# Kernel optimization log

Measured on AMD Instinct MI355X. Metric: run time of the kernel, lower is better.

## Reference

```python
import jax, jax.numpy as jnp
import numpy as np


def setup_inputs() -> dict:
    key = jax.random.key(0)
    k1, k2 = jax.random.split(key, 2)
    B, N, D = 8, 2048, 1024
    x = jax.random.normal(k1, (B, N, D), dtype=jnp.float32)
    # Linear(D, 3D): weight stored as [in, out] for x @ W
    W_qkv = jax.random.normal(k2, (D, 3 * D), dtype=jnp.float32) * (D ** -0.5)
    b_qkv = jnp.zeros((3 * D,), dtype=jnp.float32)
    return {"x": x, "W_qkv": W_qkv, "b_qkv": b_qkv}


def reference(x, W_qkv, b_qkv):
    D = x.shape[-1]
    scale = D ** -0.5
    qkv = x @ W_qkv + b_qkv                      # [B, N, 3D]
    q, k, v = jnp.split(qkv, 3, axis=-1)         # each [B, N, D]
    # attention scores: note original scales AFTER matmul (same math)
    atten = jnp.einsum('bnd,bmd->bnm', q, k) * scale  # [B, N, N]
    atten = jax.nn.softmax(atten, axis=-1)
    out = jnp.einsum('bnm,bmd->bnd', atten, v)   # [B, N, D]
    return out
```

## Files before the change

kernel.cpp:

```cpp
#include <hip/hip_runtime.h>
#include <hip/hip_bf16.h>


typedef __attribute__((ext_vector_type(8))) short bf16x8;
typedef __attribute__((ext_vector_type(4))) float f32x4;
typedef __attribute__((ext_vector_type(8))) unsigned short u16x8;
typedef __attribute__((address_space(1))) const unsigned int gu32;
typedef __attribute__((address_space(3))) unsigned int lu32;

__device__ __forceinline__ unsigned short f2bf(float f) {
  union { float f; unsigned int u; } v; v.f = f;
  unsigned int r = v.u + 0x7fffu + ((v.u >> 16) & 1u);
  return (unsigned short)(r >> 16);
}
__device__ __forceinline__ void cp16(const unsigned short* g, unsigned short* l) {
  __builtin_amdgcn_global_load_lds((gu32*)g, (lu32*)l, 16, 0, 0);
}

__global__ __launch_bounds__(256) void prep(const float* __restrict__ x,
                                            unsigned short* __restrict__ xb,
                                            const float* __restrict__ W,
                                            unsigned short* __restrict__ Wt,
                                            float* __restrict__ rowsum) {
  __shared__ unsigned short tile[64][72];
  int bid = blockIdx.x, t = threadIdx.x;
  if (bid < 8192) {
    long i = ((long)bid * 256 + t) * 8;
    float4 a = *(const float4*)(x + i);
    float4 b = *(const float4*)(x + i + 4);
    u16x8 o;
    o[0] = f2bf(a.x); o[1] = f2bf(a.y); o[2] = f2bf(a.z); o[3] = f2bf(a.w);
    o[4] = f2bf(b.x); o[5] = f2bf(b.y); o[6] = f2bf(b.z); o[7] = f2bf(b.w);
    *(u16x8*)(xb + i) = o;
  } else if (bid < 8960) {
    int wb = bid - 8192;
    int fb = wb % 48, db = wb / 48;
#pragma unroll
    for (int it = 0; it < 4; it++) {
      int c = t + it * 256;
      int r = c >> 4, c4 = (c & 15) * 4;
      float4 v = *(const float4*)(W + (long)(db * 64 + r) * 3072 + fb * 64 + c4);
      tile[r][c4 + 0] = f2bf(v.x); tile[r][c4 + 1] = f2bf(v.y);
      tile[r][c4 + 2] = f2bf(v.z); tile[r][c4 + 3] = f2bf(v.w);
    }
    __syncthreads();
#pragma unroll
    for (int it = 0; it < 2; it++) {
      int c = t + it * 256;
      int r2 = c >> 3, k8 = (c & 7) * 8;
      u16x8 o;
#pragma unroll
      for (int j = 0; j < 8; j++) o[j] = tile[k8 + j][r2];
      *(u16x8*)(Wt + (long)(fb * 64 + r2) * 1024 + db * 64 + k8) = o;
    }
  } else {
    rowsum[(bid - 8960) * 256 + t] = 0.f;
  }
}

template <int MODE, int SWZ>
__global__ __launch_bounds__(512, 2) void gemm256(
    const unsigned short* __restrict__ A, const unsigned short* __restrict__ B,
    float* __restrict__ C, const float* __restrict__ bias, int Ncols, int K, float scale,
    unsigned short* __restrict__ qp, unsigned short* __restrict__ kp,
    unsigned short* __restrict__ vp, float* __restrict__ rsum,
    long strA, long strB, long strC) {
  __shared__ __align__(16) unsigned short As[2][256 * 64];
  __shared__ __align__(16) unsigned short Bs[2][256 * 64];
  const int tid = threadIdx.x;
  const int lane = tid & 63, wave = tid >> 6;
  const int quad = lane >> 4, l16 = lane & 15;
  const int lr = lane >> 3, lc = lane & 7;
  const int bz = blockIdx.z;
  int mt, nt;
  if (SWZ == 0) {
    mt = blockIdx.y; nt = blockIdx.x;
  } else {
    int bid = blockIdx.x;
    int w = bid & 15, st = bid >> 4;
    constexpr int NSUP = (SWZ >= 4) ? (SWZ / 4) : 1;
    mt = (st / NSUP) * 4 + (w >> 2);
    nt = (st % NSUP) * 4 + (w & 3);
  }
  const long m0 = (long)mt * 256;
  const int n0 = nt * 256;
  const int wm128 = (wave >> 2) * 128;
  const int wn64 = (wave & 3) * 64;
  const int NT = K >> 6, mask = NT - 1;

  const unsigned short* __restrict__ Ab = A + (long)bz * strA;
  const unsigned short* __restrict__ Bb = B + (long)bz * strB;

  unsigned int aSrc[4], bSrc[4];
  int aOff[4], bOff[4];
  {
    const int auL[4] = {0, 128, 64, 192}, auH[4] = {32, 160, 96, 224};
    const int buL[4] = {0, 128, 32, 160}, buH[4] = {64, 192, 96, 224};
    const bool wlo = wave < 4;
    const int w8 = (wave & 3) * 8;
    const int sc = (lc ^ lr) * 8;
#pragma unroll
    for (int u = 0; u < 4; u++) {
      int ra = (wlo ? auL[u] : auH[u]) + w8 + lr;
      int rb = (wlo ? buL[u] : buH[u]) + w8 + lr;
      aSrc[u] = (unsigned int)(((int)m0 + ra) * K + sc);
      bSrc[u] = (unsigned int)((n0 + rb) * K + sc);
      aOff[u] = ra * 64 + lc * 8;
      bOff[u] = rb * 64 + lc * 8;
    }
  }

#define SA(u, bb, tt) cp16(Ab + aSrc[u] + (tt) * 64, &As[bb][aOff[u]])
#define SB(u, bb, tt) cp16(Bb + bSrc[u] + (tt) * 64, &Bs[bb][bOff[u]])

  f32x4 acc[8][4];
  f32x4 zero = {0.f, 0.f, 0.f, 0.f};
#pragma unroll
  for (int i = 0; i < 8; i++)
#pragma unroll
    for (int j = 0; j < 4; j++) acc[i][j] = zero;
  bf16x8 am[2][2][2];
  bf16x8 bn[4][2];

#define RD_AQ(d, bb, q)                                                                     \
  _Pragma("unroll") for (int ii = 0; ii < 2; ii++) {                                        \
    int row = wm128 + ((q) * 2 + ii) * 16 + l16;                                            \
    _Pragma("unroll") for (int h = 0; h < 2; h++)                                           \
      am[d][ii][h] = *(const bf16x8*)(&As[bb][row * 64 + ((((h << 2) | quad)) ^ (row & 7)) * 8]); \
  }
#define RD_BALL(bb)                                                                         \
  _Pragma("unroll") for (int jj = 0; jj < 4; jj++) {                                        \
    int row = wn64 + jj * 16 + l16;                                                         \
    _Pragma("unroll") for (int h = 0; h < 2; h++)                                           \
      bn[jj][h] = *(const bf16x8*)(&Bs[bb][row * 64 + ((((h << 2) | quad)) ^ (row & 7)) * 8]); \
  }
#define MMQ(q, d)                                                                           \
  _Pragma("unroll") for (int ii = 0; ii < 2; ii++)                                          \
    _Pragma("unroll") for (int jj = 0; jj < 4; jj++)                                        \
      _Pragma("unroll") for (int h = 0; h < 2; h++)                                         \
        acc[(q) * 2 + ii][jj] = __builtin_amdgcn_mfma_f32_16x16x32_bf16(                    \
            am[d][ii][h], bn[jj][h], acc[(q) * 2 + ii][jj], 0, 0, 0);
#define ABAR asm volatile("s_barrier" ::: "memory")
#define LGKM0 asm volatile("s_waitcnt lgkmcnt(0)" ::: "memory")
#define VMCNT4 asm volatile("s_waitcnt vmcnt(4)" ::: "memory")
#define PRIO1 __builtin_amdgcn_s_setprio(1)
#define PRIO0 __builtin_amdgcn_s_setprio(0)

#define TILE(bb, tt)                                                                        \
  {                                                                                         \
    const int t2_ = ((tt) + 2) & mask;                                                      \
                                                                                    \
    LGKM0; RD_AQ(1, bb, 1); ABAR;                                                           \
    SB(0, bb, t2_); SB(1, bb, t2_);                                                         \
    PRIO1; MMQ(0, 0); PRIO0;                                                                \
                                                                                    \
    LGKM0; RD_AQ(0, bb, 2); ABAR;                                                           \
    SA(0, bb, t2_); SA(1, bb, t2_);                                                         \
    PRIO1; MMQ(1, 1); PRIO0;                                                                \
                                                                                    \
    LGKM0; RD_AQ(1, bb, 3); VMCNT4; ABAR;                                                   \
    SB(2, bb, t2_); SB(3, bb, t2_);                                                         \
    PRIO1; MMQ(2, 0); PRIO0;                                                                \
                                                                                    \
    LGKM0; RD_AQ(0, (bb) ^ 1, 0);                                                           \
    PRIO1; MMQ(3, 1); PRIO0;                                                                \
    RD_BALL((bb) ^ 1);                                                                      \
    ABAR;                                                                                   \
    SA(2, bb, t2_); SA(3, bb, t2_);                                                         \
  }

  SA(0, 0, 0); SA(1, 0, 0); SB(0, 0, 0); SB(1, 0, 0);
  SA(2, 0, 0); SA(3, 0, 0); SB(2, 0, 0); SB(3, 0, 0);
  SA(0, 1, 1); SA(1, 1, 1); SB(0, 1, 1); SB(1, 1, 1);
  SA(2, 1, 1); SA(3, 1, 1); SB(2, 1, 1); SB(3, 1, 1);
  asm volatile("s_waitcnt vmcnt(8)" ::: "memory");
  ABAR;
  RD_AQ(0, 0, 0);
  RD_BALL(0);

#pragma unroll 1
  for (int t = 0; t < NT; t += 2) {
    TILE(0, t);
    TILE(1, t + 1);
  }

  if (MODE == 1) {
#pragma unroll
    for (int j = 0; j < 4; j++) {
      int fg = n0 + wn64 + j * 16 + l16;
      float bv = bias[fg];
      if (fg < 2048) {
        unsigned short* outp = (fg < 1024) ? qp : kp;
        int fo = fg & 1023;
#pragma unroll
        for (int i = 0; i < 8; i++)
#pragma unroll
          for (int r = 0; r < 4; r++) {
            long trow = m0 + wm128 + i * 16 + quad * 4 + r;
            outp[trow * 1024 + fo] = f2bf(acc[i][j][r] + bv);
          }
      } else {
        int d = fg - 2048;
#pragma unroll
        for (int i = 0; i < 8; i++)
#pragma unroll
          for (int r = 0; r < 4; r++) {
            long trow = m0 + wm128 + i * 16 + quad * 4 + r;
            vp[((long)(trow >> 11) * 1024 + d) * 2048 + (trow & 2047)] = f2bf(acc[i][j][r] + bv);
          }
      }
    }
  } else if (MODE == 3) {
    unsigned short* Co = qp + (long)bz * strC;
    float* rs = rsum + bz * 2048;
#pragma unroll
    for (int i = 0; i < 8; i++)
#pragma unroll
      for (int r = 0; r < 4; r++) {
        long gm = m0 + wm128 + i * 16 + quad * 4 + r;
        float psum = 0.f;
#pragma unroll
        for (int j = 0; j < 4; j++) {
          float e = __expf(acc[i][j][r] * scale);
          psum += e;
          Co[gm * Ncols + n0 + wn64 + j * 16 + l16] = f2bf(e);
        }
        psum += __shfl_xor(psum, 1);
        psum += __shfl_xor(psum, 2);
        psum += __shfl_xor(psum, 4);
        psum += __shfl_xor(psum, 8);
        if (l16 == 0) atomicAdd(rs + gm, psum);
      }
  } else {
    float* Co = C + (long)bz * strC;
    const float* rs = rsum + bz * 2048;
#pragma unroll
    for (int i = 0; i < 8; i++)
#pragma unroll
      for (int r = 0; r < 4; r++) {
        long gm = m0 + wm128 + i * 16 + quad * 4 + r;
        float inv = 1.0f / rs[gm];
#pragma unroll
        for (int j = 0; j < 4; j++)
          Co[gm * Ncols + n0 + wn64 + j * 16 + l16] = acc[i][j][r] * inv;
      }
  }
  asm volatile("s_waitcnt vmcnt(0) lgkmcnt(0)" ::: "memory");
#undef SA
#undef SB
#undef RD_AQ
#undef RD_BALL
#undef MMQ
#undef TILE
#undef ABAR
#undef LGKM0
#undef VMCNT4
#undef PRIO1
#undef PRIO0
}

extern "C" void kernel_launch(void* const* d_in, const int* in_sizes, int n_in,
                              void* d_out, int out_size, void* d_ws, size_t ws_size,
                              hipStream_t stream) {
  const float* x = (const float*)d_in[0];
  const float* W = (const float*)d_in[1];
  const float* bq = (const float*)d_in[2];
  float* out = (float*)d_out;
  char* ws = (char*)d_ws;
  const long MB = 1L << 20;
  unsigned short* Q  = (unsigned short*)(ws);
  unsigned short* Kb = (unsigned short*)(ws + 32 * MB);
  unsigned short* Vt = (unsigned short*)(ws + 64 * MB);
  unsigned short* xb = (unsigned short*)(ws + 96 * MB);
  unsigned short* Wt = (unsigned short*)(ws + 128 * MB);
  unsigned short* E  = (unsigned short*)(ws + 96 * MB);
  float* rowsum      = (float*)(ws + 160 * MB);

  prep<<<9024, 256, 0, stream>>>(x, xb, W, Wt, rowsum);
  gemm256<1, 12><<<dim3(768, 1, 1), 512, 0, stream>>>(xb, Wt, nullptr, bq, 3072, 1024, 1.0f,
                                                      Q, Kb, Vt, nullptr, 0, 0, 0);
  gemm256<3, 8><<<dim3(64, 1, 8), 512, 0, stream>>>(Q, Kb, nullptr, nullptr, 2048, 1024,
                                                    0.03125f, E, nullptr, nullptr, rowsum,
                                                    2048L * 1024, 2048L * 1024, 2048L * 2048);
  gemm256<4, 4><<<dim3(32, 1, 8), 512, 0, stream>>>(E, Vt, out, nullptr, 1024, 2048, 1.0f,
                                                    nullptr, nullptr, nullptr, rowsum,
                                                    2048L * 2048, 1024L * 2048, 2048L * 1024);
}
```

Baseline: 381.9 us.

## Write V row-major from QKV GEMM and transpose in separate kernel; remap block order

```diff
diff --git a/kernel.cpp b/kernel.cpp
--- a/kernel.cpp
+++ b/kernel.cpp
@@ -55,6 +55,34 @@
     }
   } else {
     rowsum[(bid - 8960) * 256 + t] = 0.f;
+  }
+}
+
+__global__ __launch_bounds__(256) void vtr(const unsigned short* __restrict__ V,
+                                           unsigned short* __restrict__ Vt) {
+  __shared__ unsigned short tile[64][72];
+  const int n0 = blockIdx.x * 64;
+  const int d0 = blockIdx.y * 64;
+  const int t = threadIdx.x;
+#pragma unroll
+  for (int it = 0; it < 2; it++) {
+    int idx = t + it * 256;
+    int r = idx >> 3, c8 = (idx & 7) * 8;
+    u16x8 v = *(const u16x8*)(V + (long)(n0 + r) * 1024 + d0 + c8);
+#pragma unroll
+    for (int j = 0; j < 8; j++) tile[r][c8 + j] = v[j];
+  }
+  __syncthreads();
+  const long b = n0 >> 11;
+  const int nn0 = n0 & 2047;
+#pragma unroll
+  for (int it = 0; it < 2; it++) {
+    int idx = t + it * 256;
+    int r2 = idx >> 3, k8 = (idx & 7) * 8;
+    u16x8 o;
+#pragma unroll
+    for (int j = 0; j < 8; j++) o[j] = tile[k8 + j][r2];
+    *(u16x8*)(Vt + (b * 1024 + d0 + r2) * 2048 + nn0 + k8) = o;
   }
 }
 
@@ -77,6 +105,8 @@
     mt = blockIdx.y; nt = blockIdx.x;
   } else {
     int bid = blockIdx.x;
+    const int nx = gridDim.x;
+    bid = (bid & 7) * (nx >> 3) + (bid >> 3);
     int w = bid & 15, st = bid >> 4;
     constexpr int NSUP = (SWZ >= 4) ? (SWZ / 4) : 1;
     mt = (st / NSUP) * 4 + (w >> 2);
@@ -189,26 +219,15 @@
     for (int j = 0; j < 4; j++) {
       int fg = n0 + wn64 + j * 16 + l16;
       float bv = bias[fg];
-      if (fg < 2048) {
-        unsigned short* outp = (fg < 1024) ? qp : kp;
-        int fo = fg & 1023;
-#pragma unroll
-        for (int i = 0; i < 8; i++)
-#pragma unroll
-          for (int r = 0; r < 4; r++) {
-            long trow = m0 + wm128 + i * 16 + quad * 4 + r;
-            outp[trow * 1024 + fo] = f2bf(acc[i][j][r] + bv);
-          }
-      } else {
-        int d = fg - 2048;
-#pragma unroll
-        for (int i = 0; i < 8; i++)
-#pragma unroll
-          for (int r = 0; r < 4; r++) {
-            long trow = m0 + wm128 + i * 16 + quad * 4 + r;
-            vp[((long)(trow >> 11) * 1024 + d) * 2048 + (trow & 2047)] = f2bf(acc[i][j][r] + bv);
-          }
-      }
+      unsigned short* outp = (fg < 1024) ? qp : ((fg < 2048) ? kp : vp);
+      int fo = fg & 1023;
+#pragma unroll
+      for (int i = 0; i < 8; i++)
+#pragma unroll
+        for (int r = 0; r < 4; r++) {
+          long trow = m0 + wm128 + i * 16 + quad * 4 + r;
+          outp[trow * 1024 + fo] = f2bf(acc[i][j][r] + bv);
+        }
     }
   } else if (MODE == 3) {
     unsigned short* Co = qp + (long)bz * strC;
@@ -270,15 +289,17 @@
   const long MB = 1L << 20;
   unsigned short* Q  = (unsigned short*)(ws);
   unsigned short* Kb = (unsigned short*)(ws + 32 * MB);
-  unsigned short* Vt = (unsigned short*)(ws + 64 * MB);
+  unsigned short* V  = (unsigned short*)(ws + 64 * MB);
   unsigned short* xb = (unsigned short*)(ws + 96 * MB);
   unsigned short* Wt = (unsigned short*)(ws + 128 * MB);
-  unsigned short* E  = (unsigned short*)(ws + 96 * MB);
+  unsigned short* Vt = (unsigned short*)(ws + 128 * MB);
+  unsigned short* E  = (unsigned short*)(ws + 64 * MB);
   float* rowsum      = (float*)(ws + 160 * MB);
 
   prep<<<9024, 256, 0, stream>>>(x, xb, W, Wt, rowsum);
   gemm256<1, 12><<<dim3(768, 1, 1), 512, 0, stream>>>(xb, Wt, nullptr, bq, 3072, 1024, 1.0f,
-                                                      Q, Kb, Vt, nullptr, 0, 0, 0);
+                                                      Q, Kb, V, nullptr, 0, 0, 0);
+  vtr<<<dim3(256, 16, 1), 256, 0, stream>>>(V, Vt);
   gemm256<3, 8><<<dim3(64, 1, 8), 512, 0, stream>>>(Q, Kb, nullptr, nullptr, 2048, 1024,
                                                     0.03125f, E, nullptr, nullptr, rowsum,
                                                     2048L * 1024, 2048L * 1024, 2048L * 2048);
```

Result: slower. 411.2 us (+7.7%).

## Stage bf16 GEMM epilogues through LDS for coalesced 16-byte stores

Applied to the files above, without the earlier changes.

```diff
diff --git a/kernel.cpp b/kernel.cpp
--- a/kernel.cpp
+++ b/kernel.cpp
@@ -65,18 +65,17 @@
     unsigned short* __restrict__ qp, unsigned short* __restrict__ kp,
     unsigned short* __restrict__ vp, float* __restrict__ rsum,
     long strA, long strB, long strC) {
-  __shared__ __align__(16) unsigned short As[2][256 * 64];
-  __shared__ __align__(16) unsigned short Bs[2][256 * 64];
+  __shared__ __align__(16) unsigned short smem[4][256 * 64];
   const int tid = threadIdx.x;
   const int lane = tid & 63, wave = tid >> 6;
   const int quad = lane >> 4, l16 = lane & 15;
   const int lr = lane >> 3, lc = lane & 7;
   const int bz = blockIdx.z;
   int mt, nt;
-  if (SWZ == 0) {
-    mt = blockIdx.y; nt = blockIdx.x;
-  } else {
+  {
     int bid = blockIdx.x;
+    const int nx = gridDim.x;
+    bid = (bid & 7) * (nx >> 3) + (bid >> 3);
     int w = bid & 15, st = bid >> 4;
     constexpr int NSUP = (SWZ >= 4) ? (SWZ / 4) : 1;
     mt = (st / NSUP) * 4 + (w >> 2);
@@ -110,8 +109,8 @@
     }
   }
 
-#define SA(u, bb, tt) cp16(Ab + aSrc[u] + (tt) * 64, &As[bb][aOff[u]])
-#define SB(u, bb, tt) cp16(Bb + bSrc[u] + (tt) * 64, &Bs[bb][bOff[u]])
+#define SA(u, bb, tt) cp16(Ab + aSrc[u] + (tt) * 64, &smem[bb][aOff[u]])
+#define SB(u, bb, tt) cp16(Bb + bSrc[u] + (tt) * 64, &smem[2 + (bb)][bOff[u]])
 
   f32x4 acc[8][4];
   f32x4 zero = {0.f, 0.f, 0.f, 0.f};
@@ -126,13 +125,13 @@
   _Pragma("unroll") for (int ii = 0; ii < 2; ii++) {                                        \
     int row = wm128 + ((q) * 2 + ii) * 16 + l16;                                            \
     _Pragma("unroll") for (int h = 0; h < 2; h++)                                           \
-      am[d][ii][h] = *(const bf16x8*)(&As[bb][row * 64 + ((((h << 2) | quad)) ^ (row & 7)) * 8]); \
+      am[d][ii][h] = *(const bf16x8*)(&smem[bb][row * 64 + ((((h << 2) | quad)) ^ (row & 7)) * 8]); \
   }
 #define RD_BALL(bb)                                                                         \
   _Pragma("unroll") for (int jj = 0; jj < 4; jj++) {                                        \
     int row = wn64 + jj * 16 + l16;                                                         \
     _Pragma("unroll") for (int h = 0; h < 2; h++)                                           \
-      bn[jj][h] = *(const bf16x8*)(&Bs[bb][row * 64 + ((((h << 2) | quad)) ^ (row & 7)) * 8]); \
+      bn[jj][h] = *(const bf16x8*)(&smem[2 + (bb)][row * 64 + ((((h << 2) | quad)) ^ (row & 7)) * 8]); \
   }
 #define MMQ(q, d)                                                                           \
   _Pragma("unroll") for (int ii = 0; ii < 2; ii++)                                          \
@@ -148,7 +147,8 @@
 
 #define TILE(bb, tt)                                                                        \
   {                                                                                         \
-    const int t2_ = ((tt) + 2) & mask;                                                      \
+    const int t2c_ = (tt) + 2;                                                              \
+    const int t2_ = t2c_ > mask ? mask : t2c_;                                              \
                                                                                     \
     LGKM0; RD_AQ(1, bb, 1); ABAR;                                                           \
     SB(0, bb, t2_); SB(1, bb, t2_);                                                         \
@@ -184,53 +184,70 @@
     TILE(1, t + 1);
   }
 
-  if (MODE == 1) {
-#pragma unroll
-    for (int j = 0; j < 4; j++) {
-      int fg = n0 + wn64 + j * 16 + l16;
-      float bv = bias[fg];
-      if (fg < 2048) {
-        unsigned short* outp = (fg < 1024) ? qp : kp;
-        int fo = fg & 1023;
-#pragma unroll
-        for (int i = 0; i < 8; i++)
-#pragma unroll
-          for (int r = 0; r < 4; r++) {
-            long trow = m0 + wm128 + i * 16 + quad * 4 + r;
-            outp[trow * 1024 + fo] = f2bf(acc[i][j][r] + bv);
+  if (MODE == 1 || MODE == 3) {
+    asm volatile("s_waitcnt vmcnt(0)" ::: "memory");
+    __syncthreads();
+    unsigned short* Cs = &smem[0][0];
+    if (MODE == 1) {
+      float bv[4];
+#pragma unroll
+      for (int j = 0; j < 4; j++) bv[j] = bias[n0 + wn64 + j * 16 + l16];
+      const bool isV = (n0 >= 2048);
+#pragma unroll
+      for (int i = 0; i < 8; i++)
+#pragma unroll
+        for (int r = 0; r < 4; r++) {
+          int rw = wm128 + i * 16 + quad * 4 + r;
+#pragma unroll
+          for (int j = 0; j < 4; j++) {
+            int cl = wn64 + j * 16 + l16;
+            unsigned short hv = f2bf(acc[i][j][r] + bv[j]);
+            int row = isV ? cl : rw, col = isV ? rw : cl;
+            *(unsigned short*)((char*)Cs + ((row * 512 + col * 2) ^ ((row & 7) << 4))) = hv;
           }
-      } else {
-        int d = fg - 2048;
-#pragma unroll
-        for (int i = 0; i < 8; i++)
-#pragma unroll
-          for (int r = 0; r < 4; r++) {
-            long trow = m0 + wm128 + i * 16 + quad * 4 + r;
-            vp[((long)(trow >> 11) * 1024 + d) * 2048 + (trow & 2047)] = f2bf(acc[i][j][r] + bv);
+        }
+    } else {
+      float* rs = rsum + bz * 2048;
+#pragma unroll
+      for (int i = 0; i < 8; i++)
+#pragma unroll
+        for (int r = 0; r < 4; r++) {
+          int rw = wm128 + i * 16 + quad * 4 + r;
+          float psum = 0.f;
+#pragma unroll
+          for (int j = 0; j < 4; j++) {
+            float e = __expf(acc[i][j][r] * scale);
+            psum += e;
+            int col = wn64 + j * 16 + l16;
+            *(unsigned short*)((char*)Cs + ((rw * 512 + col * 2) ^ ((rw & 7) << 4))) = f2bf(e);
           }
-      }
-    }
-  } else if (MODE == 3) {
-    unsigned short* Co = qp + (long)bz * strC;
-    float* rs = rsum + bz * 2048;
-#pragma unroll
-    for (int i = 0; i < 8; i++)
-#pragma unroll
-      for (int r = 0; r < 4; r++) {
-        long gm = m0 + wm128 + i * 16 + quad * 4 + r;
-        float psum = 0.f;
-#pragma unroll
-        for (int j = 0; j < 4; j++) {
-          float e = __expf(acc[i][j][r] * scale);
-          psum += e;
-          Co[gm * Ncols + n0 + wn64 + j * 16 + l16] = f2bf(e);
+          psum += __shfl_xor(psum, 1);
+          psum += __shfl_xor(psum, 2);
+          psum += __shfl_xor(psum, 4);
+          psum += __shfl_xor(psum, 8);
+          if (l16 == 0) atomicAdd(rs + (m0 + rw), psum);
         }
-        psum += __shfl_xor(psum, 1);
-        psum += __shfl_xor(psum, 2);
-        psum += __shfl_xor(psum, 4);
-        psum += __shfl_xor(psum, 8);
-        if (l16 == 0) atomicAdd(rs + gm, psum);
-      }
+    }
+    __syncthreads();
+    const int rrow = tid >> 5, rchunk = tid & 31;
+    unsigned short* dst;
+    long rowstr, rowbase, colbase;
+    if (MODE == 3) {
+      dst = qp + (long)bz * strC;
+      rowstr = Ncols; rowbase = m0; colbase = n0;
+    } else if (n0 < 2048) {
+      dst = (n0 < 1024) ? qp : kp;
+      rowstr = 1024; rowbase = m0; colbase = n0 & 1023;
+    } else {
+      dst = vp;
+      rowstr = 2048; rowbase = (m0 >> 11) * 1024 + (n0 - 2048); colbase = m0 & 2047;
+    }
+#pragma unroll
+    for (int k = 0; k < 16; k++) {
+      int row = k * 16 + rrow;
+      u16x8 v = *(const u16x8*)((char*)Cs + ((row * 512 + rchunk * 16) ^ ((row & 7) << 4)));
+      *(u16x8*)(dst + (rowbase + row) * rowstr + colbase + rchunk * 8) = v;
+    }
   } else {
     float* Co = C + (long)bz * strC;
     const float* rs = rsum + bz * 2048;
```

After: 369.6 us. 3.2% less time.
